# Kernel tuning notes

Hardware: AMD Instinct MI355X
Metric: run time of the kernel (lower is better)

## Reference

```python
import jax
import jax.numpy as jnp
from jax import lax
import numpy as np

NUM_LABELS = 128
PAD, BOS, EOS = 0, 1, 2
B, T = 512, 512
NEG = -10000.0


def setup_inputs() -> dict:
    key = jax.random.key(0)
    k1, k2, k3, k4 = jax.random.split(key, 4)
    features = jax.random.normal(k1, (B, T, NUM_LABELS), dtype=jnp.float32)
    tag_seqs = jax.random.randint(k2, (B, T), 0, NUM_LABELS, dtype=jnp.int32)
    # prefix-valid mask with variable lengths in [T//2, T]
    lengths = jax.random.randint(k3, (B,), T // 2, T + 1, dtype=jnp.int32)
    mask = jnp.arange(T, dtype=jnp.int32)[None, :] < lengths[:, None]
    # transitions: randn then the constrained rows/cols from CRF.__init__
    tr = jax.random.normal(k4, (NUM_LABELS, NUM_LABELS), dtype=jnp.float32)
    tr = tr.at[:, BOS].set(NEG)
    tr = tr.at[EOS, :].set(NEG)
    tr = tr.at[PAD, :].set(NEG)
    tr = tr.at[:, PAD].set(NEG)
    tr = tr.at[PAD, PAD].set(0.0)
    tr = tr.at[PAD, EOS].set(0.0)
    return {"features": features, "tag_seqs": tag_seqs, "mask": mask, "transitions": tr}


def _crf_nll(features, transitions, tag_seqs, mask):
    maskf = mask.astype(features.dtype)  # [B,T]
    # ---- gold path score (score_sentences), fully vectorized over time ----
    emis = jnp.take_along_axis(features, tag_seqs[..., None], axis=-1)[..., 0]  # [B,T]
    trans_steps = transitions[tag_seqs[:, :-1], tag_seqs[:, 1:]]               # [B,T-1]
    gold = emis[:, 0] + transitions[BOS, tag_seqs[:, 0]]
    gold = gold + jnp.sum(maskf[:, 1:] * (emis[:, 1:] + trans_steps), axis=1)
    vlen = jnp.sum(mask.astype(jnp.int32), axis=1) - 1                          # [B]
    last_lab = jnp.take_along_axis(tag_seqs, vlen[:, None], axis=1)[:, 0]
    gold = gold + transitions[last_lab, EOS]
    # ---- log-partition (forward_alg): sequential scan over time ----
    init = transitions[BOS, :][None, :] + features[:, 0]  # [B,L]

    def step(fv, xs):
        feat_t, m_t = xs  # [B,L], [B] bool
        # scores[b, prev, cur] = fv[b,prev] + trans[prev,cur] + emit[b,cur]
        scores = fv[:, :, None] + transitions[None, :, :] + feat_t[:, None, :]
        new_fv = jax.nn.logsumexp(scores, axis=1)  # [B,L]
        fv = jnp.where(m_t[:, None], new_fv, fv)
        return fv, None

    xs = (jnp.swapaxes(features[:, 1:], 0, 1), jnp.swapaxes(mask[:, 1:], 0, 1))
    fv, _ = lax.scan(step, init, xs)
    logZ = jax.nn.logsumexp(fv + transitions[:, EOS][None, :], axis=-1)  # [B]
    return -jnp.mean(gold - logZ)


def reference(features, tag_seqs, mask, transitions):
    return _crf_nll(features, transitions, tag_seqs, mask)
```

## Files before the change

kernel.cpp:

```cpp
#include <hip/hip_runtime.h>
#include <cstdint>
#include <cstddef>

#define NLAB 128
#define TT   512
#define BB   512
#define MB   16
#define PAD_ 0
#define BOS_ 1
#define EOS_ 2
#define LN2F 0.6931471805599453f

typedef float f32x4 __attribute__((ext_vector_type(4)));
typedef short s16x8 __attribute__((ext_vector_type(8)));

__device__ __forceinline__ bool mask_is_i32(const unsigned char* m8) {
    return m8[1] == 0;
}
__device__ __forceinline__ bool mask_at(const unsigned char* m8, int idx, bool isi) {
    if (isi) return ((const int*)m8)[idx] != 0;
    return m8[idx] != 0;
}

__device__ __forceinline__ unsigned f2bf(float f) {
    union { float f; unsigned u; } v; v.f = f;
    return (v.u + 0x7FFFu + ((v.u >> 16) & 1u)) >> 16;
}

__device__ __forceinline__ s16x8 eafrag(const float* __restrict__ tr, int kbase, int m) {
    s16x8 r;
    #pragma unroll
    for (int jj = 0; jj < 8; ++jj)
        r[jj] = (short)f2bf(__expf(tr[(kbase + jj) * NLAB + m]));
    return r;
}

__global__ __launch_bounds__(512, 2) void crf_forward(
        const float* __restrict__ feats,
        const int*   __restrict__ tags,
        const unsigned char* __restrict__ m8,
        const float* __restrict__ tr,
        float* __restrict__ gold_out,
        float* __restrict__ logZ_out) {
    const int tid  = threadIdx.x;
    const int blk  = blockIdx.x;
    const int w    = tid >> 6;
    const int l    = tid & 63;
    const int quad = l >> 4;
    const int col  = l & 15;
    const bool isi = mask_is_i32(m8);

    __shared__ __align__(16) unsigned short P16[2][2048];
    __shared__ int   scale_sh[2][MB];
    __shared__ float n_sh[MB];
    __shared__ float gsh[MB];
    __shared__ int   csh[MB];
    __shared__ int   len_sh[MB];
    __shared__ float red_s[8][MB];

    {
        const int bl = tid >> 5, sub = tid & 31;
        const int Bg = blk * MB + bl;
        const size_t fb = (size_t)Bg * TT * NLAB;
        float gp = 0.f; int cnt = 0;
        for (int tt = sub; tt < TT; tt += 32) {
            const int idx = Bg * TT + tt;
            const bool mm = mask_at(m8, idx, isi);
            cnt += mm ? 1 : 0;
            const int tg = tags[idx];
            if (tt == 0) gp += feats[fb + tg] + tr[BOS_ * NLAB + tg];
            else if (mm) gp += feats[fb + (size_t)tt * NLAB + tg]
                             + tr[tags[idx - 1] * NLAB + tg];
        }
        #pragma unroll
        for (int off = 16; off > 0; off >>= 1) {
            gp  += __shfl_xor(gp,  off, 64);
            cnt += __shfl_xor(cnt, off, 64);
        }
        if (sub == 0) { gsh[bl] = gp; csh[bl] = cnt; }
    }
    __syncthreads();
    if (tid < MB) {
        const int len = csh[tid];
        len_sh[tid] = len;
        const int Bg = blk * MB + tid;
        const int last = tags[Bg * TT + (len - 1)];
        gold_out[Bg] = gsh[tid] + tr[last * NLAB + EOS_];
        scale_sh[0][tid] = 0;
    }

    const int m_abs = w * 16 + col;
    const s16x8 Af0 = eafrag(tr, 0 * 32 + quad * 8, m_abs);
    const s16x8 Af1 = eafrag(tr, 1 * 32 + quad * 8, m_abs);
    const s16x8 Af2 = eafrag(tr, 2 * 32 + quad * 8, m_abs);
    const s16x8 Af3 = eafrag(tr, 3 * 32 + quad * 8, m_abs);

    const int mlab0 = w * 16 + quad * 4;
    const float trB0 = tr[BOS_ * NLAB + mlab0 + 0];
    const float trB1 = tr[BOS_ * NLAB + mlab0 + 1];
    const float trB2 = tr[BOS_ * NLAB + mlab0 + 2];
    const float trB3 = tr[BOS_ * NLAB + mlab0 + 3];
    const float trE0 = tr[(mlab0 + 0) * NLAB + EOS_];
    const float trE1 = tr[(mlab0 + 1) * NLAB + EOS_];
    const float trE2 = tr[(mlab0 + 2) * NLAB + EOS_];
    const float trE3 = tr[(mlab0 + 3) * NLAB + EOS_];

    const int Bg = blk * MB + col;
    const size_t fcol = (size_t)Bg * TT * NLAB + mlab0;

    const float4 f0 = *(const float4*)(feats + fcol);
    const float u0 = trB0 + f0.x, u1 = trB1 + f0.y,
                u2 = trB2 + f0.z, u3 = trB3 + f0.w;
    if (w == 0 && quad == 0) n_sh[col] = u3;
    __syncthreads();

    const int mylen = len_sh[col];
    int maxlen = 0;
    #pragma unroll
    for (int b = 0; b < MB; ++b) maxlen = max(maxlen, len_sh[b]);
    const float n0 = n_sh[col];

    float4 pf;
    pf.x = __expf(u0 - n0); pf.y = __expf(u1 - n0);
    pf.z = __expf(u2 - n0); pf.w = __expf(u3 - n0);
    float C = n0;

    const int wbase = ((w * 2 + (quad >> 1)) * 16 + col) * 8 + (quad & 1) * 4;
    {
        const unsigned lo = f2bf(pf.x) | (f2bf(pf.y) << 16);
        const unsigned hi = f2bf(pf.z) | (f2bf(pf.w) << 16);
        *(uint2*)(&P16[0][wbase]) = make_uint2(lo, hi);
    }

#define LDF(tt) (*(const float4*)(feats + fcol + (size_t)(tt) * NLAB))
    float4 fA = LDF(min(1, maxlen - 1)), fB = LDF(min(2, maxlen - 1)),
           fC = LDF(min(3, maxlen - 1)), fD = LDF(min(4, maxlen - 1)),
           fE = LDF(min(5, maxlen - 1)), fF = LDF(min(6, maxlen - 1)),
           fG = LDF(min(7, maxlen - 1)), fH = LDF(min(8, maxlen - 1));

    const f32x4 zacc = {0.f, 0.f, 0.f, 0.f};
    const s16x8* PA0 = (const s16x8*)P16[0];
    const s16x8* PA1 = (const s16x8*)P16[1];
    const int ra0 = (0 * 4 + quad) * 16 + col;
    const int ra1 = (1 * 4 + quad) * 16 + col;
    const int ra2 = (2 * 4 + quad) * 16 + col;
    const int ra3 = (3 * 4 + quad) * 16 + col;

#define STEP(ii, FR) {                                                        \
        const int t = t0 + (ii);                                              \
        __syncthreads();                                                      \
        const int pb = (t - 1) & 1;                                           \
        const int e  = scale_sh[pb][col];                                     \
        const s16x8* PA = pb ? PA1 : PA0;                                     \
        const s16x8 b0 = PA[ra0], b1 = PA[ra1], b2 = PA[ra2], b3 = PA[ra3];   \
        f32x4 acc0 = __builtin_amdgcn_mfma_f32_16x16x32_bf16(Af0, b0, zacc, 0, 0, 0); \
        acc0 = __builtin_amdgcn_mfma_f32_16x16x32_bf16(Af1, b1, acc0, 0, 0, 0);       \
        f32x4 acc1 = __builtin_amdgcn_mfma_f32_16x16x32_bf16(Af2, b2, zacc, 0, 0, 0); \
        acc1 = __builtin_amdgcn_mfma_f32_16x16x32_bf16(Af3, b3, acc1, 0, 0, 0);       \
        const f32x4 acc = acc0 + acc1;                                        \
        const bool live = t < mylen;                                          \
        const float qx = ldexpf(acc[0] * __expf(FR.x), -e);                   \
        const float qy = ldexpf(acc[1] * __expf(FR.y), -e);                   \
        const float qz = ldexpf(acc[2] * __expf(FR.z), -e);                   \
        const float qw = ldexpf(acc[3] * __expf(FR.w), -e);                   \
        if (live) { pf.x = qx; pf.y = qy; pf.z = qz; pf.w = qw;               \
                    C += (float)e * LN2F; }                                   \
        const unsigned lo = f2bf(pf.x) | (f2bf(pf.y) << 16);                  \
        const unsigned hi = f2bf(pf.z) | (f2bf(pf.w) << 16);                  \
        *(uint2*)(&P16[t & 1][wbase]) = make_uint2(lo, hi);                   \
        if (w == 0 && quad == 0) {                                            \
            const int se = (int)((__float_as_uint(pf.w) >> 23) & 255u) - 126; \
            scale_sh[t & 1][col] = se;                                        \
        }                                                                     \
    }

    for (int t0 = 1; t0 < maxlen; t0 += 8) {
        const int nstep = min(8, maxlen - t0);
        if (nstep > 0) STEP(0, fA)
        if (nstep > 1) STEP(1, fB)
        if (nstep > 2) STEP(2, fC)
        if (nstep > 3) STEP(3, fD)
        if (nstep > 4) STEP(4, fE)
        if (nstep > 5) STEP(5, fF)
        if (nstep > 6) STEP(6, fG)
        if (nstep > 7) STEP(7, fH)
        if (t0 + 8 < maxlen) {
            const int mx = maxlen - 1;
            fA = LDF(min(t0 + 8,  mx)); fB = LDF(min(t0 + 9,  mx));
            fC = LDF(min(t0 + 10, mx)); fD = LDF(min(t0 + 11, mx));
            fE = LDF(min(t0 + 12, mx)); fF = LDF(min(t0 + 13, mx));
            fG = LDF(min(t0 + 14, mx)); fH = LDF(min(t0 + 15, mx));
        }
    }
#undef STEP
#undef LDF

    float s = pf.x * __expf(trE0) + pf.y * __expf(trE1)
            + pf.z * __expf(trE2) + pf.w * __expf(trE3);
    s += __shfl_xor(s, 16, 64);
    s += __shfl_xor(s, 32, 64);
    if (l < 16) red_s[w][col] = s;
    __syncthreads();
    if (tid < MB) {
        float S = 0.f;
        #pragma unroll
        for (int ww = 0; ww < 8; ++ww) S += red_s[ww][tid];
        logZ_out[blk * MB + tid] = C + __logf(S);
    }
}

__global__ void crf_finalize(const float* __restrict__ gold,
                             const float* __restrict__ logZ,
                             float* __restrict__ out) {
    __shared__ float sh[4];
    const int i = threadIdx.x;
    float v = (logZ[i] - gold[i]) + (logZ[i + 256] - gold[i + 256]);
    #pragma unroll
    for (int off = 32; off > 0; off >>= 1)
        v += __shfl_xor(v, off, 64);
    if ((i & 63) == 0) sh[i >> 6] = v;
    __syncthreads();
    if (i == 0) out[0] = (sh[0] + sh[1] + sh[2] + sh[3]) * (1.0f / (float)BB);
}

extern "C" void kernel_launch(void* const* d_in, const int* in_sizes, int n_in,
                              void* d_out, int out_size, void* d_ws, size_t ws_size,
                              hipStream_t stream) {
    const float*         feats = (const float*)d_in[0];
    const int*           tags  = (const int*)d_in[1];
    const unsigned char* m8    = (const unsigned char*)d_in[2];
    const float*         tr    = (const float*)d_in[3];

    float* gold = (float*)d_ws;
    float* logZ = gold + BB;
    float* out  = (float*)d_out;

    hipLaunchKernelGGL(crf_forward,  dim3(BB / MB), dim3(512), 0, stream,
                       feats, tags, m8, tr, gold, logZ);
    hipLaunchKernelGGL(crf_finalize, dim3(1), dim3(256), 0, stream,
                       gold, logZ, out);
}
```

Before: 476.7 us.

## Run CRF forward recursion in a single wavefront per batch tile

```diff
diff --git a/kernel.cpp b/kernel.cpp
--- a/kernel.cpp
+++ b/kernel.cpp
@@ -9,10 +9,17 @@
 #define PAD_ 0
 #define BOS_ 1
 #define EOS_ 2
-#define LN2F 0.6931471805599453f
+#define LN2F  0.6931471805599453f
+#define LOG2E 1.4426950408889634f
 
 typedef float f32x4 __attribute__((ext_vector_type(4)));
 typedef short s16x8 __attribute__((ext_vector_type(8)));
+
+#if __has_builtin(__builtin_amdgcn_exp2f)
+#define EXP2F(x) __builtin_amdgcn_exp2f(x)
+#else
+#define EXP2F(x) exp2f(x)
+#endif
 
 __device__ __forceinline__ bool mask_is_i32(const unsigned char* m8) {
     return m8[1] == 0;
@@ -26,45 +33,29 @@
     union { float f; unsigned u; } v; v.f = f;
     return (v.u + 0x7FFFu + ((v.u >> 16) & 1u)) >> 16;
 }
-
-__device__ __forceinline__ s16x8 eafrag(const float* __restrict__ tr, int kbase, int m) {
-    s16x8 r;
-    #pragma unroll
-    for (int jj = 0; jj < 8; ++jj)
-        r[jj] = (short)f2bf(__expf(tr[(kbase + jj) * NLAB + m]));
+__device__ __forceinline__ unsigned cvtpk(float lo, float hi) {
+    unsigned r;
+    asm("v_cvt_pk_bf16_f32 %0, %1, %2" : "=v"(r) : "v"(lo), "v"(hi));
     return r;
 }
 
-__global__ __launch_bounds__(512, 2) void crf_forward(
+__global__ __launch_bounds__(64, 1) void crf_fused(
         const float* __restrict__ feats,
         const int*   __restrict__ tags,
         const unsigned char* __restrict__ m8,
         const float* __restrict__ tr,
         float* __restrict__ gold_out,
         float* __restrict__ logZ_out) {
-    const int tid  = threadIdx.x;
-    const int blk  = blockIdx.x;
-    const int w    = tid >> 6;
-    const int l    = tid & 63;
-    const int quad = l >> 4;
-    const int col  = l & 15;
+    const int bx  = blockIdx.x;
     const bool isi = mask_is_i32(m8);
 
-    __shared__ __align__(16) unsigned short P16[2][2048];
-    __shared__ int   scale_sh[2][MB];
-    __shared__ float n_sh[MB];
-    __shared__ float gsh[MB];
-    __shared__ int   csh[MB];
-    __shared__ int   len_sh[MB];
-    __shared__ float red_s[8][MB];
-
-    {
-        const int bl = tid >> 5, sub = tid & 31;
-        const int Bg = blk * MB + bl;
-        const size_t fb = (size_t)Bg * TT * NLAB;
+    if (bx >= BB / MB) {
+        const int b    = bx - BB / MB;
+        const int lane = threadIdx.x;
+        const size_t fb = (size_t)b * TT * NLAB;
         float gp = 0.f; int cnt = 0;
-        for (int tt = sub; tt < TT; tt += 32) {
-            const int idx = Bg * TT + tt;
+        for (int tt = lane; tt < TT; tt += 64) {
+            const int idx = b * TT + tt;
             const bool mm = mask_at(m8, idx, isi);
             cnt += mm ? 1 : 0;
             const int tg = tags[idx];
@@ -73,140 +64,165 @@
                              + tr[tags[idx - 1] * NLAB + tg];
         }
         #pragma unroll
-        for (int off = 16; off > 0; off >>= 1) {
+        for (int off = 32; off > 0; off >>= 1) {
             gp  += __shfl_xor(gp,  off, 64);
             cnt += __shfl_xor(cnt, off, 64);
         }
-        if (sub == 0) { gsh[bl] = gp; csh[bl] = cnt; }
-    }
-    __syncthreads();
-    if (tid < MB) {
-        const int len = csh[tid];
-        len_sh[tid] = len;
-        const int Bg = blk * MB + tid;
-        const int last = tags[Bg * TT + (len - 1)];
-        gold_out[Bg] = gsh[tid] + tr[last * NLAB + EOS_];
-        scale_sh[0][tid] = 0;
-    }
-
-    const int m_abs = w * 16 + col;
-    const s16x8 Af0 = eafrag(tr, 0 * 32 + quad * 8, m_abs);
-    const s16x8 Af1 = eafrag(tr, 1 * 32 + quad * 8, m_abs);
-    const s16x8 Af2 = eafrag(tr, 2 * 32 + quad * 8, m_abs);
-    const s16x8 Af3 = eafrag(tr, 3 * 32 + quad * 8, m_abs);
-
-    const int mlab0 = w * 16 + quad * 4;
-    const float trB0 = tr[BOS_ * NLAB + mlab0 + 0];
-    const float trB1 = tr[BOS_ * NLAB + mlab0 + 1];
-    const float trB2 = tr[BOS_ * NLAB + mlab0 + 2];
-    const float trB3 = tr[BOS_ * NLAB + mlab0 + 3];
-    const float trE0 = tr[(mlab0 + 0) * NLAB + EOS_];
-    const float trE1 = tr[(mlab0 + 1) * NLAB + EOS_];
-    const float trE2 = tr[(mlab0 + 2) * NLAB + EOS_];
-    const float trE3 = tr[(mlab0 + 3) * NLAB + EOS_];
-
-    const int Bg = blk * MB + col;
-    const size_t fcol = (size_t)Bg * TT * NLAB + mlab0;
-
-    const float4 f0 = *(const float4*)(feats + fcol);
-    const float u0 = trB0 + f0.x, u1 = trB1 + f0.y,
-                u2 = trB2 + f0.z, u3 = trB3 + f0.w;
-    if (w == 0 && quad == 0) n_sh[col] = u3;
-    __syncthreads();
-
-    const int mylen = len_sh[col];
-    int maxlen = 0;
-    #pragma unroll
-    for (int b = 0; b < MB; ++b) maxlen = max(maxlen, len_sh[b]);
-    const float n0 = n_sh[col];
-
-    float4 pf;
-    pf.x = __expf(u0 - n0); pf.y = __expf(u1 - n0);
-    pf.z = __expf(u2 - n0); pf.w = __expf(u3 - n0);
-    float C = n0;
-
-    const int wbase = ((w * 2 + (quad >> 1)) * 16 + col) * 8 + (quad & 1) * 4;
+        if (lane == 0)
+            gold_out[b] = gp + tr[tags[b * TT + cnt - 1] * NLAB + EOS_];
+        return;
+    }
+
+    const int tid = threadIdx.x;
+    const int a   = tid >> 4;
+    const int c   = tid & 15;
+    const int G   = bx * MB + c;
+
+    __shared__ __align__(16) unsigned short P16[2][2048];
+
+    int cnt = 0;
+    if (isi) {
+        const uint4* mp = (const uint4*)((const int*)m8 + (size_t)G * TT + a * 128);
+        #pragma unroll 8
+        for (int i = 0; i < 32; ++i) {
+            uint4 v = mp[i];
+            cnt += (v.x != 0) + (v.y != 0) + (v.z != 0) + (v.w != 0);
+        }
+    } else {
+        const uint4* mp = (const uint4*)(m8 + (size_t)G * TT + a * 128);
+        #pragma unroll
+        for (int i = 0; i < 8; ++i) {
+            uint4 v = mp[i];
+            cnt += (int)((((v.x & 0x01010101u) * 0x01010101u) >> 24)
+                       + (((v.y & 0x01010101u) * 0x01010101u) >> 24)
+                       + (((v.z & 0x01010101u) * 0x01010101u) >> 24)
+                       + (((v.w & 0x01010101u) * 0x01010101u) >> 24));
+        }
+    }
+    cnt += __shfl_xor(cnt, 16, 64);
+    cnt += __shfl_xor(cnt, 32, 64);
+    const int mylen = cnt;
+    int maxlen = mylen;
+    maxlen = max(maxlen, __shfl_xor(maxlen, 1, 64));
+    maxlen = max(maxlen, __shfl_xor(maxlen, 2, 64));
+    maxlen = max(maxlen, __shfl_xor(maxlen, 4, 64));
+    maxlen = max(maxlen, __shfl_xor(maxlen, 8, 64));
+    const int mx = maxlen - 1;
+
+    const size_t fbase = (size_t)G * TT * NLAB;
+
+    f32x4 F0[8], F1[8];
     {
-        const unsigned lo = f2bf(pf.x) | (f2bf(pf.y) << 16);
-        const unsigned hi = f2bf(pf.z) | (f2bf(pf.w) << 16);
-        *(uint2*)(&P16[0][wbase]) = make_uint2(lo, hi);
-    }
-
-#define LDF(tt) (*(const float4*)(feats + fcol + (size_t)(tt) * NLAB))
-    float4 fA = LDF(min(1, maxlen - 1)), fB = LDF(min(2, maxlen - 1)),
-           fC = LDF(min(3, maxlen - 1)), fD = LDF(min(4, maxlen - 1)),
-           fE = LDF(min(5, maxlen - 1)), fF = LDF(min(6, maxlen - 1)),
-           fG = LDF(min(7, maxlen - 1)), fH = LDF(min(8, maxlen - 1));
-
+        const f32x4* fp1 = (const f32x4*)(feats + fbase + (size_t)min(1, mx) * NLAB);
+        const f32x4* fp2 = (const f32x4*)(feats + fbase + (size_t)min(2, mx) * NLAB);
+        #pragma unroll
+        for (int mt = 0; mt < 8; ++mt) { F1[mt] = fp1[4 * mt + a]; F0[mt] = fp2[4 * mt + a]; }
+    }
+
+    s16x8 Af[8][4];
+    #pragma unroll
+    for (int kt = 0; kt < 4; ++kt)
+        #pragma unroll
+        for (int jj = 0; jj < 8; ++jj) {
+            const float* tp = tr + (kt * 32 + a * 8 + jj) * NLAB + c;
+            #pragma unroll
+            for (int mt = 0; mt < 8; ++mt)
+                Af[mt][kt][jj] = (short)f2bf(__expf(tp[mt * 16]));
+        }
+
+    f32x4 pf[8];
+    float C;
+    {
+        f32x4 u[8];
+        #pragma unroll
+        for (int mt = 0; mt < 8; ++mt) {
+            const f32x4 tb = *(const f32x4*)(tr + BOS_ * NLAB + mt * 16 + a * 4);
+            const f32x4 ff = *(const f32x4*)(feats + fbase + mt * 16 + a * 4);
+            u[mt] = tb + ff;
+        }
+        const float n0 = __shfl(u[0][3], c, 64);
+        C = n0;
+        #pragma unroll
+        for (int mt = 0; mt < 8; ++mt)
+            #pragma unroll
+            for (int r = 0; r < 4; ++r)
+                pf[mt][r] = __expf(u[mt][r] - n0);
+    }
+
+    const int rab = a * 16 + c;
+    #pragma unroll
+    for (int mt = 0; mt < 8; ++mt) {
+        const unsigned lo = cvtpk(pf[mt][0], pf[mt][1]);
+        const unsigned hi = cvtpk(pf[mt][2], pf[mt][3]);
+        *(uint2*)&P16[0][((2 * mt + (a >> 1)) * 16 + c) * 8 + (a & 1) * 4]
+            = make_uint2(lo, hi);
+    }
+    int e_cur = 0;
     const f32x4 zacc = {0.f, 0.f, 0.f, 0.f};
-    const s16x8* PA0 = (const s16x8*)P16[0];
-    const s16x8* PA1 = (const s16x8*)P16[1];
-    const int ra0 = (0 * 4 + quad) * 16 + col;
-    const int ra1 = (1 * 4 + quad) * 16 + col;
-    const int ra2 = (2 * 4 + quad) * 16 + col;
-    const int ra3 = (3 * 4 + quad) * 16 + col;
-
-#define STEP(ii, FR) {                                                        \
-        const int t = t0 + (ii);                                              \
-        __syncthreads();                                                      \
-        const int pb = (t - 1) & 1;                                           \
-        const int e  = scale_sh[pb][col];                                     \
-        const s16x8* PA = pb ? PA1 : PA0;                                     \
-        const s16x8 b0 = PA[ra0], b1 = PA[ra1], b2 = PA[ra2], b3 = PA[ra3];   \
-        f32x4 acc0 = __builtin_amdgcn_mfma_f32_16x16x32_bf16(Af0, b0, zacc, 0, 0, 0); \
-        acc0 = __builtin_amdgcn_mfma_f32_16x16x32_bf16(Af1, b1, acc0, 0, 0, 0);       \
-        f32x4 acc1 = __builtin_amdgcn_mfma_f32_16x16x32_bf16(Af2, b2, zacc, 0, 0, 0); \
-        acc1 = __builtin_amdgcn_mfma_f32_16x16x32_bf16(Af3, b3, acc1, 0, 0, 0);       \
-        const f32x4 acc = acc0 + acc1;                                        \
-        const bool live = t < mylen;                                          \
-        const float qx = ldexpf(acc[0] * __expf(FR.x), -e);                   \
-        const float qy = ldexpf(acc[1] * __expf(FR.y), -e);                   \
-        const float qz = ldexpf(acc[2] * __expf(FR.z), -e);                   \
-        const float qw = ldexpf(acc[3] * __expf(FR.w), -e);                   \
-        if (live) { pf.x = qx; pf.y = qy; pf.z = qz; pf.w = qw;               \
-                    C += (float)e * LN2F; }                                   \
-        const unsigned lo = f2bf(pf.x) | (f2bf(pf.y) << 16);                  \
-        const unsigned hi = f2bf(pf.z) | (f2bf(pf.w) << 16);                  \
-        *(uint2*)(&P16[t & 1][wbase]) = make_uint2(lo, hi);                   \
-        if (w == 0 && quad == 0) {                                            \
-            const int se = (int)((__float_as_uint(pf.w) >> 23) & 255u) - 126; \
-            scale_sh[t & 1][col] = se;                                        \
+
+#define STEP(tcur, PBR, PBW, FF) {                                            \
+    const int t_ = (tcur);                                                    \
+    const bool live = t_ < mylen;                                             \
+    const s16x8* PR = (const s16x8*)P16[PBR];                                 \
+    const s16x8 b0 = PR[rab],       b1 = PR[64  + rab],                       \
+                b2 = PR[128 + rab], b3 = PR[192 + rab];                       \
+    f32x4 acc[8];                                                             \
+    _Pragma("unroll")                                                         \
+    for (int mt = 0; mt < 8; ++mt) {                                          \
+        f32x4 a0 = __builtin_amdgcn_mfma_f32_16x16x32_bf16(Af[mt][0], b0, zacc, 0, 0, 0); \
+        a0 = __builtin_amdgcn_mfma_f32_16x16x32_bf16(Af[mt][1], b1, a0, 0, 0, 0);         \
+        f32x4 a1 = __builtin_amdgcn_mfma_f32_16x16x32_bf16(Af[mt][2], b2, zacc, 0, 0, 0); \
+        a1 = __builtin_amdgcn_mfma_f32_16x16x32_bf16(Af[mt][3], b3, a1, 0, 0, 0);         \
+        acc[mt] = a0 + a1;                                                    \
+    }                                                                         \
+      \
+    const float ef_ = (float)e_cur;                                           \
+    f32x4 ef2[8];                                                             \
+    _Pragma("unroll")                                                         \
+    for (int mt = 0; mt < 8; ++mt)                                            \
+        _Pragma("unroll")                                                     \
+        for (int r = 0; r < 4; ++r)                                           \
+            ef2[mt][r] = EXP2F(__builtin_fmaf(FF[mt][r], LOG2E, -ef_));       \
+           \
+    {                                                                         \
+        const int tl = min(t_ + 2, mx);                                       \
+        const f32x4* fp = (const f32x4*)(feats + fbase + (size_t)tl * NLAB);  \
+        _Pragma("unroll")                                                     \
+        for (int mt = 0; mt < 8; ++mt) FF[mt] = fp[4 * mt + a];               \
+    }                                                                         \
+    _Pragma("unroll")                                                         \
+    for (int mt = 0; mt < 8; ++mt) {                                          \
+        _Pragma("unroll")                                                     \
+        for (int r = 0; r < 4; ++r) {                                         \
+            const float q = acc[mt][r] * ef2[mt][r];                          \
+            if (live) pf[mt][r] = q;                                          \
         }                                                                     \
-    }
-
-    for (int t0 = 1; t0 < maxlen; t0 += 8) {
-        const int nstep = min(8, maxlen - t0);
-        if (nstep > 0) STEP(0, fA)
-        if (nstep > 1) STEP(1, fB)
-        if (nstep > 2) STEP(2, fC)
-        if (nstep > 3) STEP(3, fD)
-        if (nstep > 4) STEP(4, fE)
-        if (nstep > 5) STEP(5, fF)
-        if (nstep > 6) STEP(6, fG)
-        if (nstep > 7) STEP(7, fH)
-        if (t0 + 8 < maxlen) {
-            const int mx = maxlen - 1;
-            fA = LDF(min(t0 + 8,  mx)); fB = LDF(min(t0 + 9,  mx));
-            fC = LDF(min(t0 + 10, mx)); fD = LDF(min(t0 + 11, mx));
-            fE = LDF(min(t0 + 12, mx)); fF = LDF(min(t0 + 13, mx));
-            fG = LDF(min(t0 + 14, mx)); fH = LDF(min(t0 + 15, mx));
-        }
+        const unsigned lo = cvtpk(pf[mt][0], pf[mt][1]);                      \
+        const unsigned hi = cvtpk(pf[mt][2], pf[mt][3]);                      \
+        *(uint2*)&P16[PBW][((2 * mt + (a >> 1)) * 16 + c) * 8 + (a & 1) * 4]  \
+            = make_uint2(lo, hi);                                             \
+    }                                                                         \
+    if (live) C += (float)e_cur * LN2F;                                       \
+    const int se = (int)((__float_as_uint(pf[0][3]) >> 23) & 255u) - 126;     \
+    e_cur = __shfl(se, c, 64);      \
+}
+
+    #pragma unroll 1
+    for (int t0 = 1; t0 < maxlen; t0 += 2) {
+        STEP(t0,     0, 1, F1)
+        STEP(t0 + 1, 1, 0, F0)
     }
 #undef STEP
-#undef LDF
-
-    float s = pf.x * __expf(trE0) + pf.y * __expf(trE1)
-            + pf.z * __expf(trE2) + pf.w * __expf(trE3);
+
+    float s = 0.f;
+    #pragma unroll
+    for (int mt = 0; mt < 8; ++mt)
+        #pragma unroll
+        for (int r = 0; r < 4; ++r)
+            s += pf[mt][r] * __expf(tr[(mt * 16 + a * 4 + r) * NLAB + EOS_]);
     s += __shfl_xor(s, 16, 64);
     s += __shfl_xor(s, 32, 64);
-    if (l < 16) red_s[w][col] = s;
-    __syncthreads();
-    if (tid < MB) {
-        float S = 0.f;
-        #pragma unroll
-        for (int ww = 0; ww < 8; ++ww) S += red_s[ww][tid];
-        logZ_out[blk * MB + tid] = C + __logf(S);
-    }
+    if (tid < 16) logZ_out[G] = C + __logf(s);
 }
 
 __global__ void crf_finalize(const float* __restrict__ gold,
@@ -235,7 +251,7 @@
     float* logZ = gold + BB;
     float* out  = (float*)d_out;
 
-    hipLaunchKernelGGL(crf_forward,  dim3(BB / MB), dim3(512), 0, stream,
+    hipLaunchKernelGGL(crf_fused, dim3(BB / MB + BB), dim3(64), 0, stream,
                        feats, tags, m8, tr, gold, logZ);
     hipLaunchKernelGGL(crf_finalize, dim3(1), dim3(256), 0, stream,
                        gold, logZ, out);
```

Result: slower. 635.9 us (+33.4%).
